# Kernel tuning notes

Hardware: AMD Instinct MI355X
Metric: run time of the kernel (lower is better)

The kernel has to match this reference:

```python
import jax, jax.numpy as jnp
import numpy as np

N_NODES = 100000
N_EDGES = 1600000
INPUT_DIM = 128
HIDDEN = 128
OUTPUT_DIM = 2
NUM_LAYERS = 2
MAX_RECURSION = 10
TAU_THRESHOLD = 0.005


def setup_inputs() -> dict:
    key = jax.random.key(0)
    ks = jax.random.split(key, 16)
    s = 0.05
    x = jax.random.normal(ks[0], (N_NODES, INPUT_DIM), dtype=jnp.float32)
    edge_index = jax.random.randint(ks[1], (2, N_EDGES), 0, N_NODES, dtype=jnp.int64)
    W_in = jax.random.normal(ks[2], (HIDDEN, INPUT_DIM), dtype=jnp.float32) * s
    b_in = jax.random.normal(ks[3], (HIDDEN,), dtype=jnp.float32) * s
    Wd = jax.random.normal(ks[4], (NUM_LAYERS, HIDDEN, 2 * HIDDEN), dtype=jnp.float32) * s
    bd = jax.random.normal(ks[5], (NUM_LAYERS, HIDDEN), dtype=jnp.float32) * s
    Wt = jax.random.normal(ks[6], (1, HIDDEN), dtype=jnp.float32) * s
    bt = jax.random.normal(ks[7], (1,), dtype=jnp.float32) * s
    W_ih = jax.random.normal(ks[8], (3 * HIDDEN, HIDDEN), dtype=jnp.float32) * s
    W_hh = jax.random.normal(ks[9], (3 * HIDDEN, HIDDEN), dtype=jnp.float32) * s
    b_ih = jax.random.normal(ks[10], (3 * HIDDEN,), dtype=jnp.float32) * s
    b_hh = jax.random.normal(ks[11], (3 * HIDDEN,), dtype=jnp.float32) * s
    Wo = jax.random.normal(ks[12], (OUTPUT_DIM, HIDDEN), dtype=jnp.float32) * s
    bo = jax.random.normal(ks[13], (OUTPUT_DIM,), dtype=jnp.float32) * s
    return dict(x=x, edge_index=edge_index, W_in=W_in, b_in=b_in, Wd=Wd, bd=bd,
                Wt=Wt, bt=bt, W_ih=W_ih, W_hh=W_hh, b_ih=b_ih, b_hh=b_hh, Wo=Wo, bo=bo)


def _gru_cell(x, h, W_ih, W_hh, b_ih, b_hh):
    # torch.nn.GRUCell math
    gi = x @ W_ih.T + b_ih  # [N, 3H]
    gh = h @ W_hh.T + b_hh
    i_r, i_z, i_n = jnp.split(gi, 3, axis=-1)
    h_r, h_z, h_n = jnp.split(gh, 3, axis=-1)
    r = jax.nn.sigmoid(i_r + h_r)
    z = jax.nn.sigmoid(i_z + h_z)
    n = jnp.tanh(i_n + r * h_n)
    return (1.0 - z) * n + z * h


def reference(x, edge_index, W_in, b_in, Wd, bd, Wt, bt, W_ih, W_hh, b_ih, b_hh, Wo, bo):
    N = x.shape[0]
    row, col = edge_index[0], edge_index[1]
    h = jax.nn.relu(x @ W_in.T + b_in)  # [N, H]
    tau = None
    for l in range(NUM_LAYERS):
        diff = jnp.abs(h[row] - h[col])  # [E, H]
        diff_agg = jax.ops.segment_sum(diff, row, num_segments=N)  # [N, H]
        h = jax.nn.relu(jnp.concatenate([h, diff_agg], axis=-1) @ Wd[l].T + bd[l])
        tau = jax.nn.softplus(h @ Wt.T + bt).squeeze(-1)  # [N]
        # n_updates = clamp(floor(1/tau), max=MAX_RECURSION); node updated iff
        # n_updates > 0 and tau < TAU_THRESHOLD. The original inner loop applies
        # gru(diff_agg[i], h[i]) with the ORIGINAL h[i] each iteration, so repeated
        # application is idempotent -> single masked GRU step is exact same math.
        n_updates = jnp.minimum(jnp.floor(1.0 / tau).astype(jnp.int32), MAX_RECURSION)
        mask = (n_updates > 0) & (tau < TAU_THRESHOLD)
        h_gru = _gru_cell(diff_agg, h, W_ih, W_hh, b_ih, b_hh)
        h = jnp.where(mask[:, None], h_gru, h)
    out = h @ Wo.T + bo  # [N, OUTPUT_DIM]
    return out, tau
```

## Files before the change

### kernel.cpp

```cpp
#include <hip/hip_runtime.h>
#include <cstdint>
#include <cstddef>

#define HID 128
#define BSHIFT 7
#define NSB 256
#define MAXB 4096

__global__ __launch_bounds__(256)
void ecount_kernel(const int* __restrict__ row, int* __restrict__ countsT,
                   int E, int nbuck,
                   const float* __restrict__ W_in, const float* __restrict__ Wd,
                   const float* __restrict__ W_ih, const float* __restrict__ W_hh,
                   float* __restrict__ WinT, float* __restrict__ WdT0,
                   float* __restrict__ WdT1, float* __restrict__ WihT,
                   float* __restrict__ WhhT) {
  for (int i = blockIdx.x * 256 + threadIdx.x; i < 180224; i += NSB * 256) {
    int j = i;
    if (j < 16384) { int r = j >> 7, c = j & 127; WinT[c * 128 + r] = W_in[j]; continue; }
    j -= 16384;
    if (j < 32768) { int r = j >> 8, c = j & 255; WdT0[c * 128 + r] = Wd[j]; continue; }
    j -= 32768;
    if (j < 32768) { int r = j >> 8, c = j & 255; WdT1[c * 128 + r] = Wd[32768 + j]; continue; }
    j -= 32768;
    if (j < 49152) { int r = j >> 7, c = j & 127; WihT[c * 384 + r] = W_ih[j]; continue; }
    j -= 49152;
    { int r = j >> 7, c = j & 127; WhhT[c * 384 + r] = W_hh[j]; }
  }
  __shared__ int lh[1024];
  int b = blockIdx.x;
  for (int i = threadIdx.x; i < nbuck; i += 256) lh[i] = 0;
  __syncthreads();
  int per = (E + NSB - 1) / NSB;
  int s = b * per, e = min(s + per, E);
  for (int i = s + (int)threadIdx.x; i < e; i += 256)
    atomicAdd(&lh[row[i] >> BSHIFT], 1);
  __syncthreads();
  for (int i = threadIdx.x; i < nbuck; i += 256) countsT[i * NSB + b] = lh[i];
}

__global__ __launch_bounds__(NSB)
void bprefix_kernel(int* __restrict__ countsT, int* __restrict__ btotal, int nbuck) {
  __shared__ int sd[NSB];
  int bk = blockIdx.x;
  int t = threadIdx.x;
  int v = countsT[bk * NSB + t];
  sd[t] = v;
  __syncthreads();
  for (int off = 1; off < NSB; off <<= 1) {
    int u = (t >= off) ? sd[t - off] : 0;
    __syncthreads();
    sd[t] += u;
    __syncthreads();
  }
  countsT[bk * NSB + t] = sd[t] - v;
  if (t == NSB - 1) btotal[bk] = sd[t];
}

__global__ __launch_bounds__(1024)
void bstart_kernel(const int* __restrict__ btotal, int* __restrict__ bstart,
                   int* __restrict__ offsets, int N, int nbuck) {
  __shared__ int sd[1024];
  int t = threadIdx.x;
  int v = (t < nbuck) ? btotal[t] : 0;
  sd[t] = v;
  __syncthreads();
  for (int off = 1; off < 1024; off <<= 1) {
    int u = (t >= off) ? sd[t - off] : 0;
    __syncthreads();
    sd[t] += u;
    __syncthreads();
  }
  if (t < nbuck) bstart[t] = sd[t] - v;
  if (t == nbuck - 1) { bstart[nbuck] = sd[t]; offsets[N] = sd[t]; }
}

__global__ __launch_bounds__(256)
void escatter_kernel(const int* __restrict__ row, const int* __restrict__ col,
                     const int* __restrict__ countsT, const int* __restrict__ bstart,
                     int2* __restrict__ ebuf, int E, int nbuck) {
  __shared__ int lcur[1024];
  int b = blockIdx.x;
  for (int i = threadIdx.x; i < nbuck; i += 256)
    lcur[i] = bstart[i] + countsT[i * NSB + b];
  __syncthreads();
  int per = (E + NSB - 1) / NSB;
  int s = b * per, e = min(s + per, E);
  for (int i = s + (int)threadIdx.x; i < e; i += 256) {
    int r = row[i], c = col[i];
    int pos = atomicAdd(&lcur[r >> BSHIFT], 1);
    ebuf[pos] = make_int2(r, c);
  }
}

__global__ __launch_bounds__(256)
void bsort_kernel(const int2* __restrict__ ebuf, const int* __restrict__ bstart,
                  int* __restrict__ offsets, int* __restrict__ csr_col,
                  int N, int nbuck) {
  __shared__ int cnt[128], off[128], cur[128];
  __shared__ int lcol[MAXB];
  int bk = blockIdx.x;
  int tid = threadIdx.x;
  int s = bstart[bk], e = bstart[bk + 1];
  int m = e - s;
  if (tid < 128) cnt[tid] = 0;
  __syncthreads();
  for (int i = s + tid; i < e; i += 256)
    atomicAdd(&cnt[ebuf[i].x & 127], 1);
  __syncthreads();
  if (tid < 128) off[tid] = cnt[tid];
  __syncthreads();
  for (int d = 1; d < 128; d <<= 1) {
    int v = 0;
    if (tid < 128 && tid >= d) v = off[tid - d];
    __syncthreads();
    if (tid < 128) off[tid] += v;
    __syncthreads();
  }
  if (tid < 128) {
    cur[tid] = off[tid] - cnt[tid];
    int node = (bk << BSHIFT) + tid;
    if (node < N) offsets[node] = s + off[tid] - cnt[tid];
  }
  __syncthreads();
  if (m <= MAXB) {
    for (int i = s + tid; i < e; i += 256) {
      int2 rc = ebuf[i];
      int pos = atomicAdd(&cur[rc.x & 127], 1);
      lcol[pos] = rc.y;
    }
    __syncthreads();
    if (tid < 128) {
      int b0 = off[tid] - cnt[tid], b1 = off[tid];
      for (int i = b0 + 1; i < b1; ++i) {
        int key = lcol[i];
        int j = i - 1;
        while (j >= b0 && lcol[j] > key) { lcol[j + 1] = lcol[j]; --j; }
        lcol[j + 1] = key;
      }
    }
    __syncthreads();
    for (int i = tid; i < m; i += 256) csr_col[s + i] = lcol[i];
  } else {
    for (int i = s + tid; i < e; i += 256) {
      int2 rc = ebuf[i];
      int pos = atomicAdd(&cur[rc.x & 127], 1);
      csr_col[s + pos] = rc.y;
    }
  }
}

__global__ __launch_bounds__(256)
void aggregate_kernel(const float* __restrict__ h, const int* __restrict__ offsets,
                      const int* __restrict__ csr_col, float* __restrict__ diff,
                      int N) {
  int wave = threadIdx.x >> 6;
  int lane = threadIdx.x & 63;
  int node = blockIdx.x * 4 + wave;
  if (node >= N) return;
  int start = offsets[node], end = offsets[node + 1];
  int deg = end - start;
  const float2* hrow = (const float2*)(h + (size_t)node * HID);
  float2 hv = hrow[lane];
  float a0 = 0.f, a1 = 0.f;

  int batch = min(deg, 64);
  int myc = (lane < batch) ? csr_col[start + lane] : 0;
  int j = 0;
  for (; j + 16 <= batch; j += 16) {
    const float2* p0 = (const float2*)(h + (size_t)__shfl(myc, j + 0) * HID);
    const float2* p1 = (const float2*)(h + (size_t)__shfl(myc, j + 1) * HID);
    const float2* p2 = (const float2*)(h + (size_t)__shfl(myc, j + 2) * HID);
    const float2* p3 = (const float2*)(h + (size_t)__shfl(myc, j + 3) * HID);
    const float2* p4 = (const float2*)(h + (size_t)__shfl(myc, j + 4) * HID);
    const float2* p5 = (const float2*)(h + (size_t)__shfl(myc, j + 5) * HID);
    const float2* p6 = (const float2*)(h + (size_t)__shfl(myc, j + 6) * HID);
    const float2* p7 = (const float2*)(h + (size_t)__shfl(myc, j + 7) * HID);
    const float2* q0 = (const float2*)(h + (size_t)__shfl(myc, j + 8) * HID);
    const float2* q1 = (const float2*)(h + (size_t)__shfl(myc, j + 9) * HID);
    const float2* q2 = (const float2*)(h + (size_t)__shfl(myc, j + 10) * HID);
    const float2* q3 = (const float2*)(h + (size_t)__shfl(myc, j + 11) * HID);
    const float2* q4 = (const float2*)(h + (size_t)__shfl(myc, j + 12) * HID);
    const float2* q5 = (const float2*)(h + (size_t)__shfl(myc, j + 13) * HID);
    const float2* q6 = (const float2*)(h + (size_t)__shfl(myc, j + 14) * HID);
    const float2* q7 = (const float2*)(h + (size_t)__shfl(myc, j + 15) * HID);
    float2 x0 = p0[lane], x1 = p1[lane], x2 = p2[lane], x3 = p3[lane];
    float2 x4 = p4[lane], x5 = p5[lane], x6 = p6[lane], x7 = p7[lane];
    float2 y0 = q0[lane], y1 = q1[lane], y2 = q2[lane], y3 = q3[lane];
    float2 y4 = q4[lane], y5 = q5[lane], y6 = q6[lane], y7 = q7[lane];
    a0 += fabsf(hv.x - x0.x) + fabsf(hv.x - x1.x) + fabsf(hv.x - x2.x) + fabsf(hv.x - x3.x)
        + fabsf(hv.x - x4.x) + fabsf(hv.x - x5.x) + fabsf(hv.x - x6.x) + fabsf(hv.x - x7.x);
    a1 += fabsf(hv.y - x0.y) + fabsf(hv.y - x1.y) + fabsf(hv.y - x2.y) + fabsf(hv.y - x3.y)
        + fabsf(hv.y - x4.y) + fabsf(hv.y - x5.y) + fabsf(hv.y - x6.y) + fabsf(hv.y - x7.y);
    a0 += fabsf(hv.x - y0.x) + fabsf(hv.x - y1.x) + fabsf(hv.x - y2.x) + fabsf(hv.x - y3.x)
        + fabsf(hv.x - y4.x) + fabsf(hv.x - y5.x) + fabsf(hv.x - y6.x) + fabsf(hv.x - y7.x);
    a1 += fabsf(hv.y - y0.y) + fabsf(hv.y - y1.y) + fabsf(hv.y - y2.y) + fabsf(hv.y - y3.y)
        + fabsf(hv.y - y4.y) + fabsf(hv.y - y5.y) + fabsf(hv.y - y6.y) + fabsf(hv.y - y7.y);
  }
  for (; j + 8 <= batch; j += 8) {
    const float2* p0 = (const float2*)(h + (size_t)__shfl(myc, j + 0) * HID);
    const float2* p1 = (const float2*)(h + (size_t)__shfl(myc, j + 1) * HID);
    const float2* p2 = (const float2*)(h + (size_t)__shfl(myc, j + 2) * HID);
    const float2* p3 = (const float2*)(h + (size_t)__shfl(myc, j + 3) * HID);
    const float2* p4 = (const float2*)(h + (size_t)__shfl(myc, j + 4) * HID);
    const float2* p5 = (const float2*)(h + (size_t)__shfl(myc, j + 5) * HID);
    const float2* p6 = (const float2*)(h + (size_t)__shfl(myc, j + 6) * HID);
    const float2* p7 = (const float2*)(h + (size_t)__shfl(myc, j + 7) * HID);
    float2 x0 = p0[lane], x1 = p1[lane], x2 = p2[lane], x3 = p3[lane];
    float2 x4 = p4[lane], x5 = p5[lane], x6 = p6[lane], x7 = p7[lane];
    a0 += fabsf(hv.x - x0.x) + fabsf(hv.x - x1.x) + fabsf(hv.x - x2.x) + fabsf(hv.x - x3.x)
        + fabsf(hv.x - x4.x) + fabsf(hv.x - x5.x) + fabsf(hv.x - x6.x) + fabsf(hv.x - x7.x);
    a1 += fabsf(hv.y - x0.y) + fabsf(hv.y - x1.y) + fabsf(hv.y - x2.y) + fabsf(hv.y - x3.y)
        + fabsf(hv.y - x4.y) + fabsf(hv.y - x5.y) + fabsf(hv.y - x6.y) + fabsf(hv.y - x7.y);
  }
  for (; j < batch; ++j) {
    const float2* p = (const float2*)(h + (size_t)__shfl(myc, j) * HID);
    float2 x = p[lane];
    a0 += fabsf(hv.x - x.x);
    a1 += fabsf(hv.y - x.y);
  }
  for (int e = start + 64; e < end; ++e) {
    const float2* p = (const float2*)(h + (size_t)csr_col[e] * HID);
    float2 x = p[lane];
    a0 += fabsf(hv.x - x.x);
    a1 += fabsf(hv.y - x.y);
  }
  *(float2*)(diff + (size_t)node * HID + 2 * lane) = make_float2(a0, a1);
}

template<bool TAU>
__global__ __launch_bounds__(256)
void gemm_kernel(const float* __restrict__ A1, const float* __restrict__ A2,
                 const float* __restrict__ BT, const float* __restrict__ bias,
                 float* __restrict__ C, int M, int nchunks,
                 const float* __restrict__ Wt, const float* __restrict__ bt,
                 float* __restrict__ tau_out, int* __restrict__ mlist,
                 int* __restrict__ mcount) {
  __shared__ float As[32][68];
  __shared__ float Bs[32][128];
  __shared__ float taured[64];
  int tid = threadIdx.x;
  int tx = tid & 31;
  int ty = tid >> 5;
  int i0 = blockIdx.x * 64;
  float acc[8][4] = {};

  for (int kc = 0; kc < nchunks; ++kc) {
    const float* A = (kc < 4) ? A1 : A2;
    int ksrc = (kc & 3) * 32;
    int kglob = kc * 32;
    #pragma unroll
    for (int q = 0; q < 2; ++q) {
      int f = q * 256 + tid;
      int i = f >> 3;
      int kq = (f & 7) << 2;
      int ig = i0 + i; if (ig >= M) ig = M - 1;
      float4 v = *(const float4*)(A + (size_t)ig * HID + ksrc + kq);
      As[kq + 0][i] = v.x; As[kq + 1][i] = v.y;
      As[kq + 2][i] = v.z; As[kq + 3][i] = v.w;
    }
    #pragma unroll
    for (int q = 0; q < 4; ++q) {
      int f = q * 256 + tid;
      int k = f >> 5; int c4 = (f & 31) << 2;
      *(float4*)&Bs[k][c4] = *(const float4*)(BT + (size_t)(kglob + k) * HID + c4);
    }
    __syncthreads();
    #pragma unroll
    for (int k = 0; k < 32; ++k) {
      float a[8];
      const float4* ap = (const float4*)&As[k][ty * 8];
      float4 a0 = ap[0], a1 = ap[1];
      a[0]=a0.x; a[1]=a0.y; a[2]=a0.z; a[3]=a0.w;
      a[4]=a1.x; a[5]=a1.y; a[6]=a1.z; a[7]=a1.w;
      float4 b4 = *(const float4*)&Bs[k][tx * 4];
      #pragma unroll
      for (int r = 0; r < 8; ++r) {
        acc[r][0] = fmaf(a[r], b4.x, acc[r][0]);
        acc[r][1] = fmaf(a[r], b4.y, acc[r][1]);
        acc[r][2] = fmaf(a[r], b4.z, acc[r][2]);
        acc[r][3] = fmaf(a[r], b4.w, acc[r][3]);
      }
    }
    __syncthreads();
  }

  float4 bias4 = *(const float4*)(bias + tx * 4);
  float bias_r[4] = {bias4.x, bias4.y, bias4.z, bias4.w};
  float wt_r[4] = {0.f, 0.f, 0.f, 0.f};
  if constexpr (TAU) {
    float4 w4 = *(const float4*)(Wt + tx * 4);
    wt_r[0] = w4.x; wt_r[1] = w4.y; wt_r[2] = w4.z; wt_r[3] = w4.w;
  }
  #pragma unroll
  for (int r = 0; r < 8; ++r) {
    int row = i0 + ty * 8 + r;
    bool ok = row < M;
    float v0 = fmaxf(acc[r][0] + bias_r[0], 0.f);
    float v1 = fmaxf(acc[r][1] + bias_r[1], 0.f);
    float v2 = fmaxf(acc[r][2] + bias_r[2], 0.f);
    float v3 = fmaxf(acc[r][3] + bias_r[3], 0.f);
    if (ok) {
      float4 v4 = make_float4(v0, v1, v2, v3);
      *(float4*)(C + (size_t)row * HID + tx * 4) = v4;
    }
    if constexpr (TAU) {
      float p = v0 * wt_r[0];
      p = fmaf(v1, wt_r[1], p);
      p = fmaf(v2, wt_r[2], p);
      p = fmaf(v3, wt_r[3], p);
      p += __shfl_down(p, 16, 32);
      p += __shfl_down(p, 8, 32);
      p += __shfl_down(p, 4, 32);
      p += __shfl_down(p, 2, 32);
      p += __shfl_down(p, 1, 32);
      if (tx == 0) taured[ty * 8 + r] = p;
    }
  }
  if constexpr (TAU) {
    __syncthreads();
    if (tid < 64) {
      int row = i0 + tid;
      if (row < M) {
        float pre = taured[tid] + bt[0];
        float tau = (pre > 20.f) ? pre : log1pf(expf(pre));
        tau_out[row] = tau;
        if (tau < 0.005f && (1.0f / tau) < 2147483648.0f) {
          int pos = atomicAdd(mcount, 1);
          mlist[pos] = row;
        }
      }
    }
  }
}

__global__ __launch_bounds__(512)
void gru_kernel(const float* __restrict__ diff, float* __restrict__ h,
                const int* __restrict__ list, const int* __restrict__ count,
                const float* __restrict__ WihT, const float* __restrict__ WhhT,
                const float* __restrict__ b_ih, const float* __restrict__ b_hh) {
  int cnt = *count;
  int base = blockIdx.x * 32;
  if (base >= cnt) return;
  __shared__ float dl[32][HID];
  __shared__ float hl[32][HID];
  __shared__ int ids[32];
  int tid = threadIdx.x;
  if (tid < 32) ids[tid] = (base + tid < cnt) ? list[base + tid] : -1;
  __syncthreads();
  #pragma unroll
  for (int q = 0; q < 8; ++q) {
    int f = q * 512 + tid;
    int r = f >> 7, c = f & 127;
    int id = ids[r];
    int src = (id >= 0) ? id : 0;
    dl[r][c] = diff[(size_t)src * HID + c];
    hl[r][c] = h[(size_t)src * HID + c];
  }
  __syncthreads();
  int tx = tid & 127, ty = tid >> 7;
  float air[8] = {}, aiz[8] = {}, ain[8] = {}, ahr[8] = {}, ahz[8] = {}, ahn[8] = {};
  for (int k = 0; k < HID; ++k) {
    float wir = WihT[k * 384 + tx];
    float wiz = WihT[k * 384 + 128 + tx];
    float win = WihT[k * 384 + 256 + tx];
    float whr = WhhT[k * 384 + tx];
    float whz = WhhT[k * 384 + 128 + tx];
    float whn = WhhT[k * 384 + 256 + tx];
    #pragma unroll
    for (int r = 0; r < 8; ++r) {
      float dk = dl[ty * 8 + r][k];
      float hk = hl[ty * 8 + r][k];
      air[r] = fmaf(dk, wir, air[r]);
      aiz[r] = fmaf(dk, wiz, aiz[r]);
      ain[r] = fmaf(dk, win, ain[r]);
      ahr[r] = fmaf(hk, whr, ahr[r]);
      ahz[r] = fmaf(hk, whz, ahz[r]);
      ahn[r] = fmaf(hk, whn, ahn[r]);
    }
  }
  float bir = b_ih[tx], biz = b_ih[128 + tx], bin = b_ih[256 + tx];
  float bhr = b_hh[tx], bhz = b_hh[128 + tx], bhn = b_hh[256 + tx];
  #pragma unroll
  for (int r = 0; r < 8; ++r) {
    int id = ids[ty * 8 + r];
    if (id < 0) continue;
    float rg = 1.f / (1.f + expf(-((air[r] + bir) + (ahr[r] + bhr))));
    float z  = 1.f / (1.f + expf(-((aiz[r] + biz) + (ahz[r] + bhz))));
    float n  = tanhf((ain[r] + bin) + rg * (ahn[r] + bhn));
    float hv = hl[ty * 8 + r][tx];
    h[(size_t)id * HID + tx] = (1.f - z) * n + z * hv;
  }
}

__global__ void out_kernel(const float* __restrict__ h, const float* __restrict__ Wo,
                           const float* __restrict__ bo, float* __restrict__ out, int N) {
  int g = blockIdx.x * blockDim.x + threadIdx.x;
  int node = g >> 5;
  int sub = threadIdx.x & 31;
  if (node >= N) return;
  float4 hv = *(const float4*)(h + (size_t)node * HID + sub * 4);
  float4 w0 = *(const float4*)(Wo + sub * 4);
  float4 w1 = *(const float4*)(Wo + 128 + sub * 4);
  float s0 = hv.x * w0.x + hv.y * w0.y + hv.z * w0.z + hv.w * w0.w;
  float s1 = hv.x * w1.x + hv.y * w1.y + hv.z * w1.z + hv.w * w1.w;
  for (int d = 16; d; d >>= 1) {
    s0 += __shfl_down(s0, d, 32);
    s1 += __shfl_down(s1, d, 32);
  }
  if (sub == 0) {
    out[(size_t)node * 2 + 0] = s0 + bo[0];
    out[(size_t)node * 2 + 1] = s1 + bo[1];
  }
}

extern "C" void kernel_launch(void* const* d_in, const int* in_sizes, int n_in,
                              void* d_out, int out_size, void* d_ws, size_t ws_size,
                              hipStream_t stream) {
  const float* x    = (const float*)d_in[0];
  const int*   ei   = (const int*)d_in[1];
  const float* W_in = (const float*)d_in[2];
  const float* b_in = (const float*)d_in[3];
  const float* Wd   = (const float*)d_in[4];
  const float* bd   = (const float*)d_in[5];
  const float* Wt   = (const float*)d_in[6];
  const float* bt   = (const float*)d_in[7];
  const float* W_ih = (const float*)d_in[8];
  const float* W_hh = (const float*)d_in[9];
  const float* b_ih = (const float*)d_in[10];
  const float* b_hh = (const float*)d_in[11];
  const float* Wo   = (const float*)d_in[12];
  const float* bo   = (const float*)d_in[13];

  const int N = in_sizes[0] / HID;
  const int E = in_sizes[1] / 2;
  const int* rowp = ei;
  const int* colp = ei + E;
  const int nbuck = (N + (1 << BSHIFT) - 1) >> BSHIFT;

  char* p = (char*)d_ws;
  auto alloc = [&](size_t bytes) { void* r = (void*)p; p += (bytes + 255) & ~(size_t)255; return r; };
  float* hA     = (float*)alloc((size_t)N * HID * 4);
  float* hB     = (float*)alloc((size_t)N * HID * 4);
  float* diff   = (float*)alloc((size_t)N * HID * 4);
  float* WinT   = (float*)alloc(128 * 128 * 4);
  float* WdT0   = (float*)alloc(256 * 128 * 4);
  float* WdT1   = (float*)alloc(256 * 128 * 4);
  float* WihT   = (float*)alloc(128 * 384 * 4);
  float* WhhT   = (float*)alloc(128 * 384 * 4);
  float* tau0   = (float*)alloc((size_t)N * 4);
  int*   list   = (int*)alloc((size_t)N * 4);
  int*   count  = (int*)alloc(256);
  int*   countsT= (int*)alloc((size_t)1024 * NSB * 4);
  int*   btotal = (int*)alloc(1024 * 4);
  int*   bstart = (int*)alloc(1028 * 4);
  int*   offs   = (int*)alloc(((size_t)N + 1) * 4);
  int*   csrcol = (int*)alloc((size_t)E * 4);
  int2*  ebuf   = (int2*)alloc((size_t)E * 8);

  float* out_ptr = (float*)d_out;
  float* tau_out = (float*)d_out + (size_t)N * 2;

  hipMemsetAsync(count, 0, 8, stream);

  ecount_kernel<<<NSB, 256, 0, stream>>>(rowp, countsT, E, nbuck,
                                         W_in, Wd, W_ih, W_hh,
                                         WinT, WdT0, WdT1, WihT, WhhT);
  bprefix_kernel<<<nbuck, NSB, 0, stream>>>(countsT, btotal, nbuck);
  bstart_kernel<<<1, 1024, 0, stream>>>(btotal, bstart, offs, N, nbuck);
  escatter_kernel<<<NSB, 256, 0, stream>>>(rowp, colp, countsT, bstart, ebuf, E, nbuck);
  bsort_kernel<<<nbuck, 256, 0, stream>>>(ebuf, bstart, offs, csrcol, N, nbuck);

  const int gemm_blocks = (N + 63) / 64;
  const int agg_blocks = (N + 3) / 4;
  const int gru_blocks = (N + 31) / 32;

  gemm_kernel<false><<<gemm_blocks, 256, 0, stream>>>(
      x, nullptr, WinT, b_in, hA, N, 4, nullptr, nullptr, nullptr, nullptr, nullptr);

  aggregate_kernel<<<agg_blocks, 256, 0, stream>>>(hA, offs, csrcol, diff, N);
  gemm_kernel<true><<<gemm_blocks, 256, 0, stream>>>(
      hA, diff, WdT0, bd, hB, N, 8, Wt, bt, tau0, list, count);
  gru_kernel<<<gru_blocks, 512, 0, stream>>>(diff, hB, list, count, WihT, WhhT, b_ih, b_hh);

  aggregate_kernel<<<agg_blocks, 256, 0, stream>>>(hB, offs, csrcol, diff, N);
  gemm_kernel<true><<<gemm_blocks, 256, 0, stream>>>(
      hB, diff, WdT1, bd + 128, hA, N, 8, Wt, bt, tau_out, list, count + 1);
  gru_kernel<<<gru_blocks, 512, 0, stream>>>(diff, hA, list, count + 1, WihT, WhhT, b_ih, b_hh);

  out_kernel<<<((size_t)N * 32 + 255) / 256, 256, 0, stream>>>(hA, Wo, bo, out_ptr, N);
}
```

Measured before the change: 737.6 us.

## Fuse neighbor aggregation into layer GEMM and fold output projection into epilogues

The separate aggregate kernel is replaced by an aggregation phase inside each layer GEMM block: each block computes the diff rows for its 64 nodes into shared memory and uses them directly as the second half of the K dimension, so those rows no longer have to be reread from global memory. The output projection kernel is removed. It is now computed in the last layer GEMM epilogue for all nodes and recomputed in the final GRU kernel for the nodes that GRU updates. The fused kernel uses about 52KB of shared memory, which lowers occupancy during the latency-bound gather phase. Diff is still written to global memory because the GRU needs it.

Result: slower. 866.6 us (+17.5%).

```diff
diff --git a/kernel.cpp b/kernel.cpp
--- a/kernel.cpp
+++ b/kernel.cpp
@@ -6,6 +6,7 @@
 #define BSHIFT 7
 #define NSB 256
 #define MAXB 4096
+
 
 __global__ __launch_bounds__(256)
 void ecount_kernel(const int* __restrict__ row, int* __restrict__ countsT,
@@ -151,104 +152,17 @@
 }
 
 __global__ __launch_bounds__(256)
-void aggregate_kernel(const float* __restrict__ h, const int* __restrict__ offsets,
-                      const int* __restrict__ csr_col, float* __restrict__ diff,
-                      int N) {
-  int wave = threadIdx.x >> 6;
-  int lane = threadIdx.x & 63;
-  int node = blockIdx.x * 4 + wave;
-  if (node >= N) return;
-  int start = offsets[node], end = offsets[node + 1];
-  int deg = end - start;
-  const float2* hrow = (const float2*)(h + (size_t)node * HID);
-  float2 hv = hrow[lane];
-  float a0 = 0.f, a1 = 0.f;
-
-  int batch = min(deg, 64);
-  int myc = (lane < batch) ? csr_col[start + lane] : 0;
-  int j = 0;
-  for (; j + 16 <= batch; j += 16) {
-    const float2* p0 = (const float2*)(h + (size_t)__shfl(myc, j + 0) * HID);
-    const float2* p1 = (const float2*)(h + (size_t)__shfl(myc, j + 1) * HID);
-    const float2* p2 = (const float2*)(h + (size_t)__shfl(myc, j + 2) * HID);
-    const float2* p3 = (const float2*)(h + (size_t)__shfl(myc, j + 3) * HID);
-    const float2* p4 = (const float2*)(h + (size_t)__shfl(myc, j + 4) * HID);
-    const float2* p5 = (const float2*)(h + (size_t)__shfl(myc, j + 5) * HID);
-    const float2* p6 = (const float2*)(h + (size_t)__shfl(myc, j + 6) * HID);
-    const float2* p7 = (const float2*)(h + (size_t)__shfl(myc, j + 7) * HID);
-    const float2* q0 = (const float2*)(h + (size_t)__shfl(myc, j + 8) * HID);
-    const float2* q1 = (const float2*)(h + (size_t)__shfl(myc, j + 9) * HID);
-    const float2* q2 = (const float2*)(h + (size_t)__shfl(myc, j + 10) * HID);
-    const float2* q3 = (const float2*)(h + (size_t)__shfl(myc, j + 11) * HID);
-    const float2* q4 = (const float2*)(h + (size_t)__shfl(myc, j + 12) * HID);
-    const float2* q5 = (const float2*)(h + (size_t)__shfl(myc, j + 13) * HID);
-    const float2* q6 = (const float2*)(h + (size_t)__shfl(myc, j + 14) * HID);
-    const float2* q7 = (const float2*)(h + (size_t)__shfl(myc, j + 15) * HID);
-    float2 x0 = p0[lane], x1 = p1[lane], x2 = p2[lane], x3 = p3[lane];
-    float2 x4 = p4[lane], x5 = p5[lane], x6 = p6[lane], x7 = p7[lane];
-    float2 y0 = q0[lane], y1 = q1[lane], y2 = q2[lane], y3 = q3[lane];
-    float2 y4 = q4[lane], y5 = q5[lane], y6 = q6[lane], y7 = q7[lane];
-    a0 += fabsf(hv.x - x0.x) + fabsf(hv.x - x1.x) + fabsf(hv.x - x2.x) + fabsf(hv.x - x3.x)
-        + fabsf(hv.x - x4.x) + fabsf(hv.x - x5.x) + fabsf(hv.x - x6.x) + fabsf(hv.x - x7.x);
-    a1 += fabsf(hv.y - x0.y) + fabsf(hv.y - x1.y) + fabsf(hv.y - x2.y) + fabsf(hv.y - x3.y)
-        + fabsf(hv.y - x4.y) + fabsf(hv.y - x5.y) + fabsf(hv.y - x6.y) + fabsf(hv.y - x7.y);
-    a0 += fabsf(hv.x - y0.x) + fabsf(hv.x - y1.x) + fabsf(hv.x - y2.x) + fabsf(hv.x - y3.x)
-        + fabsf(hv.x - y4.x) + fabsf(hv.x - y5.x) + fabsf(hv.x - y6.x) + fabsf(hv.x - y7.x);
-    a1 += fabsf(hv.y - y0.y) + fabsf(hv.y - y1.y) + fabsf(hv.y - y2.y) + fabsf(hv.y - y3.y)
-        + fabsf(hv.y - y4.y) + fabsf(hv.y - y5.y) + fabsf(hv.y - y6.y) + fabsf(hv.y - y7.y);
-  }
-  for (; j + 8 <= batch; j += 8) {
-    const float2* p0 = (const float2*)(h + (size_t)__shfl(myc, j + 0) * HID);
-    const float2* p1 = (const float2*)(h + (size_t)__shfl(myc, j + 1) * HID);
-    const float2* p2 = (const float2*)(h + (size_t)__shfl(myc, j + 2) * HID);
-    const float2* p3 = (const float2*)(h + (size_t)__shfl(myc, j + 3) * HID);
-    const float2* p4 = (const float2*)(h + (size_t)__shfl(myc, j + 4) * HID);
-    const float2* p5 = (const float2*)(h + (size_t)__shfl(myc, j + 5) * HID);
-    const float2* p6 = (const float2*)(h + (size_t)__shfl(myc, j + 6) * HID);
-    const float2* p7 = (const float2*)(h + (size_t)__shfl(myc, j + 7) * HID);
-    float2 x0 = p0[lane], x1 = p1[lane], x2 = p2[lane], x3 = p3[lane];
-    float2 x4 = p4[lane], x5 = p5[lane], x6 = p6[lane], x7 = p7[lane];
-    a0 += fabsf(hv.x - x0.x) + fabsf(hv.x - x1.x) + fabsf(hv.x - x2.x) + fabsf(hv.x - x3.x)
-        + fabsf(hv.x - x4.x) + fabsf(hv.x - x5.x) + fabsf(hv.x - x6.x) + fabsf(hv.x - x7.x);
-    a1 += fabsf(hv.y - x0.y) + fabsf(hv.y - x1.y) + fabsf(hv.y - x2.y) + fabsf(hv.y - x3.y)
-        + fabsf(hv.y - x4.y) + fabsf(hv.y - x5.y) + fabsf(hv.y - x6.y) + fabsf(hv.y - x7.y);
-  }
-  for (; j < batch; ++j) {
-    const float2* p = (const float2*)(h + (size_t)__shfl(myc, j) * HID);
-    float2 x = p[lane];
-    a0 += fabsf(hv.x - x.x);
-    a1 += fabsf(hv.y - x.y);
-  }
-  for (int e = start + 64; e < end; ++e) {
-    const float2* p = (const float2*)(h + (size_t)csr_col[e] * HID);
-    float2 x = p[lane];
-    a0 += fabsf(hv.x - x.x);
-    a1 += fabsf(hv.y - x.y);
-  }
-  *(float2*)(diff + (size_t)node * HID + 2 * lane) = make_float2(a0, a1);
-}
-
-template<bool TAU>
-__global__ __launch_bounds__(256)
-void gemm_kernel(const float* __restrict__ A1, const float* __restrict__ A2,
-                 const float* __restrict__ BT, const float* __restrict__ bias,
-                 float* __restrict__ C, int M, int nchunks,
-                 const float* __restrict__ Wt, const float* __restrict__ bt,
-                 float* __restrict__ tau_out, int* __restrict__ mlist,
-                 int* __restrict__ mcount) {
+void gemm_in_kernel(const float* __restrict__ A, const float* __restrict__ BT,
+                    const float* __restrict__ bias, float* __restrict__ C, int M) {
   __shared__ float As[32][68];
   __shared__ float Bs[32][128];
-  __shared__ float taured[64];
   int tid = threadIdx.x;
   int tx = tid & 31;
   int ty = tid >> 5;
   int i0 = blockIdx.x * 64;
   float acc[8][4] = {};
-
-  for (int kc = 0; kc < nchunks; ++kc) {
-    const float* A = (kc < 4) ? A1 : A2;
-    int ksrc = (kc & 3) * 32;
-    int kglob = kc * 32;
+  for (int kc = 0; kc < 4; ++kc) {
+    int ksrc = kc * 32;
     #pragma unroll
     for (int q = 0; q < 2; ++q) {
       int f = q * 256 + tid;
@@ -263,7 +177,7 @@
     for (int q = 0; q < 4; ++q) {
       int f = q * 256 + tid;
       int k = f >> 5; int c4 = (f & 31) << 2;
-      *(float4*)&Bs[k][c4] = *(const float4*)(BT + (size_t)(kglob + k) * HID + c4);
+      *(float4*)&Bs[k][c4] = *(const float4*)(BT + (size_t)(ksrc + k) * HID + c4);
     }
     __syncthreads();
     #pragma unroll
@@ -284,13 +198,171 @@
     }
     __syncthreads();
   }
+  float4 bias4 = *(const float4*)(bias + tx * 4);
+  #pragma unroll
+  for (int r = 0; r < 8; ++r) {
+    int row = i0 + ty * 8 + r;
+    if (row >= M) continue;
+    float4 v4 = make_float4(fmaxf(acc[r][0] + bias4.x, 0.f),
+                            fmaxf(acc[r][1] + bias4.y, 0.f),
+                            fmaxf(acc[r][2] + bias4.z, 0.f),
+                            fmaxf(acc[r][3] + bias4.w, 0.f));
+    *(float4*)(C + (size_t)row * HID + tx * 4) = v4;
+  }
+}
+
+template<bool OUT>
+__global__ __launch_bounds__(256)
+void fgemm_kernel(const float* __restrict__ h, const float* __restrict__ BT,
+                  const float* __restrict__ bias, float* __restrict__ C,
+                  const int* __restrict__ offsets, const int* __restrict__ csr_col,
+                  float* __restrict__ diffG, int M,
+                  const float* __restrict__ Wt, const float* __restrict__ bt,
+                  float* __restrict__ tau_out, int* __restrict__ mlist,
+                  int* __restrict__ mcount,
+                  const float* __restrict__ Wo, const float* __restrict__ bo,
+                  float* __restrict__ outp) {
+  __shared__ float As[32][68];
+  __shared__ float Bs[32][128];
+  __shared__ float dL[128][68];
+  __shared__ float taured[64];
+  int tid = threadIdx.x;
+  int i0 = blockIdx.x * 64;
+
+  {
+    int wave = tid >> 6;
+    int lane = tid & 63;
+    for (int t = 0; t < 16; ++t) {
+      int nl = wave * 16 + t;
+      int node = i0 + nl;
+      if (node >= M) break;
+      int start = offsets[node], end = offsets[node + 1];
+      int deg = end - start;
+      const float2* hrow = (const float2*)(h + (size_t)node * HID);
+      float2 hv = hrow[lane];
+      float a0 = 0.f, a1 = 0.f;
+      int batch = min(deg, 64);
+      int myc = (lane < batch) ? csr_col[start + lane] : 0;
+      int j = 0;
+      for (; j + 16 <= batch; j += 16) {
+        const float2* p0 = (const float2*)(h + (size_t)__shfl(myc, j + 0) * HID);
+        const float2* p1 = (const float2*)(h + (size_t)__shfl(myc, j + 1) * HID);
+        const float2* p2 = (const float2*)(h + (size_t)__shfl(myc, j + 2) * HID);
+        const float2* p3 = (const float2*)(h + (size_t)__shfl(myc, j + 3) * HID);
+        const float2* p4 = (const float2*)(h + (size_t)__shfl(myc, j + 4) * HID);
+        const float2* p5 = (const float2*)(h + (size_t)__shfl(myc, j + 5) * HID);
+        const float2* p6 = (const float2*)(h + (size_t)__shfl(myc, j + 6) * HID);
+        const float2* p7 = (const float2*)(h + (size_t)__shfl(myc, j + 7) * HID);
+        const float2* q0 = (const float2*)(h + (size_t)__shfl(myc, j + 8) * HID);
+        const float2* q1 = (const float2*)(h + (size_t)__shfl(myc, j + 9) * HID);
+        const float2* q2 = (const float2*)(h + (size_t)__shfl(myc, j + 10) * HID);
+        const float2* q3 = (const float2*)(h + (size_t)__shfl(myc, j + 11) * HID);
+        const float2* q4 = (const float2*)(h + (size_t)__shfl(myc, j + 12) * HID);
+        const float2* q5 = (const float2*)(h + (size_t)__shfl(myc, j + 13) * HID);
+        const float2* q6 = (const float2*)(h + (size_t)__shfl(myc, j + 14) * HID);
+        const float2* q7 = (const float2*)(h + (size_t)__shfl(myc, j + 15) * HID);
+        float2 x0 = p0[lane], x1 = p1[lane], x2 = p2[lane], x3 = p3[lane];
+        float2 x4 = p4[lane], x5 = p5[lane], x6 = p6[lane], x7 = p7[lane];
+        float2 y0 = q0[lane], y1 = q1[lane], y2 = q2[lane], y3 = q3[lane];
+        float2 y4 = q4[lane], y5 = q5[lane], y6 = q6[lane], y7 = q7[lane];
+        a0 += fabsf(hv.x - x0.x) + fabsf(hv.x - x1.x) + fabsf(hv.x - x2.x) + fabsf(hv.x - x3.x)
+            + fabsf(hv.x - x4.x) + fabsf(hv.x - x5.x) + fabsf(hv.x - x6.x) + fabsf(hv.x - x7.x);
+        a1 += fabsf(hv.y - x0.y) + fabsf(hv.y - x1.y) + fabsf(hv.y - x2.y) + fabsf(hv.y - x3.y)
+            + fabsf(hv.y - x4.y) + fabsf(hv.y - x5.y) + fabsf(hv.y - x6.y) + fabsf(hv.y - x7.y);
+        a0 += fabsf(hv.x - y0.x) + fabsf(hv.x - y1.x) + fabsf(hv.x - y2.x) + fabsf(hv.x - y3.x)
+            + fabsf(hv.x - y4.x) + fabsf(hv.x - y5.x) + fabsf(hv.x - y6.x) + fabsf(hv.x - y7.x);
+        a1 += fabsf(hv.y - y0.y) + fabsf(hv.y - y1.y) + fabsf(hv.y - y2.y) + fabsf(hv.y - y3.y)
+            + fabsf(hv.y - y4.y) + fabsf(hv.y - y5.y) + fabsf(hv.y - y6.y) + fabsf(hv.y - y7.y);
+      }
+      for (; j + 8 <= batch; j += 8) {
+        const float2* p0 = (const float2*)(h + (size_t)__shfl(myc, j + 0) * HID);
+        const float2* p1 = (const float2*)(h + (size_t)__shfl(myc, j + 1) * HID);
+        const float2* p2 = (const float2*)(h + (size_t)__shfl(myc, j + 2) * HID);
+        const float2* p3 = (const float2*)(h + (size_t)__shfl(myc, j + 3) * HID);
+        const float2* p4 = (const float2*)(h + (size_t)__shfl(myc, j + 4) * HID);
+        const float2* p5 = (const float2*)(h + (size_t)__shfl(myc, j + 5) * HID);
+        const float2* p6 = (const float2*)(h + (size_t)__shfl(myc, j + 6) * HID);
+        const float2* p7 = (const float2*)(h + (size_t)__shfl(myc, j + 7) * HID);
+        float2 x0 = p0[lane], x1 = p1[lane], x2 = p2[lane], x3 = p3[lane];
+        float2 x4 = p4[lane], x5 = p5[lane], x6 = p6[lane], x7 = p7[lane];
+        a0 += fabsf(hv.x - x0.x) + fabsf(hv.x - x1.x) + fabsf(hv.x - x2.x) + fabsf(hv.x - x3.x)
+            + fabsf(hv.x - x4.x) + fabsf(hv.x - x5.x) + fabsf(hv.x - x6.x) + fabsf(hv.x - x7.x);
+        a1 += fabsf(hv.y - x0.y) + fabsf(hv.y - x1.y) + fabsf(hv.y - x2.y) + fabsf(hv.y - x3.y)
+            + fabsf(hv.y - x4.y) + fabsf(hv.y - x5.y) + fabsf(hv.y - x6.y) + fabsf(hv.y - x7.y);
+      }
+      for (; j < batch; ++j) {
+        const float2* p = (const float2*)(h + (size_t)__shfl(myc, j) * HID);
+        float2 x = p[lane];
+        a0 += fabsf(hv.x - x.x);
+        a1 += fabsf(hv.y - x.y);
+      }
+      for (int e2 = start + 64; e2 < end; ++e2) {
+        const float2* p = (const float2*)(h + (size_t)csr_col[e2] * HID);
+        float2 x = p[lane];
+        a0 += fabsf(hv.x - x.x);
+        a1 += fabsf(hv.y - x.y);
+      }
+      *(float2*)(diffG + (size_t)node * HID + 2 * lane) = make_float2(a0, a1);
+      dL[2 * lane][nl] = a0;
+      dL[2 * lane + 1][nl] = a1;
+    }
+  }
+  __syncthreads();
+
+  int tx = tid & 31;
+  int ty = tid >> 5;
+  float acc[8][4] = {};
+  for (int kc = 0; kc < 8; ++kc) {
+    if (kc < 4) {
+      int ksrc = kc * 32;
+      #pragma unroll
+      for (int q = 0; q < 2; ++q) {
+        int f = q * 256 + tid;
+        int i = f >> 3;
+        int kq = (f & 7) << 2;
+        int ig = i0 + i; if (ig >= M) ig = M - 1;
+        float4 v = *(const float4*)(h + (size_t)ig * HID + ksrc + kq);
+        As[kq + 0][i] = v.x; As[kq + 1][i] = v.y;
+        As[kq + 2][i] = v.z; As[kq + 3][i] = v.w;
+      }
+    }
+    int kglob = kc * 32;
+    #pragma unroll
+    for (int q = 0; q < 4; ++q) {
+      int f = q * 256 + tid;
+      int k = f >> 5; int c4 = (f & 31) << 2;
+      *(float4*)&Bs[k][c4] = *(const float4*)(BT + (size_t)(kglob + k) * HID + c4);
+    }
+    __syncthreads();
+    const float (*Asrc)[68] = (kc < 4) ? As : (const float (*)[68])&dL[(kc - 4) * 32];
+    #pragma unroll
+    for (int k = 0; k < 32; ++k) {
+      float a[8];
+      const float4* ap = (const float4*)&Asrc[k][ty * 8];
+      float4 a0 = ap[0], a1 = ap[1];
+      a[0]=a0.x; a[1]=a0.y; a[2]=a0.z; a[3]=a0.w;
+      a[4]=a1.x; a[5]=a1.y; a[6]=a1.z; a[7]=a1.w;
+      float4 b4 = *(const float4*)&Bs[k][tx * 4];
+      #pragma unroll
+      for (int r = 0; r < 8; ++r) {
+        acc[r][0] = fmaf(a[r], b4.x, acc[r][0]);
+        acc[r][1] = fmaf(a[r], b4.y, acc[r][1]);
+        acc[r][2] = fmaf(a[r], b4.z, acc[r][2]);
+        acc[r][3] = fmaf(a[r], b4.w, acc[r][3]);
+      }
+    }
+    __syncthreads();
+  }
 
   float4 bias4 = *(const float4*)(bias + tx * 4);
   float bias_r[4] = {bias4.x, bias4.y, bias4.z, bias4.w};
-  float wt_r[4] = {0.f, 0.f, 0.f, 0.f};
-  if constexpr (TAU) {
-    float4 w4 = *(const float4*)(Wt + tx * 4);
-    wt_r[0] = w4.x; wt_r[1] = w4.y; wt_r[2] = w4.z; wt_r[3] = w4.w;
+  float4 w4 = *(const float4*)(Wt + tx * 4);
+  float wt_r[4] = {w4.x, w4.y, w4.z, w4.w};
+  float4 wo0 = make_float4(0.f, 0.f, 0.f, 0.f);
+  float4 wo1 = make_float4(0.f, 0.f, 0.f, 0.f);
+  if constexpr (OUT) {
+    wo0 = *(const float4*)(Wo + tx * 4);
+    wo1 = *(const float4*)(Wo + 128 + tx * 4);
   }
   #pragma unroll
   for (int r = 0; r < 8; ++r) {
@@ -304,47 +376,62 @@
       float4 v4 = make_float4(v0, v1, v2, v3);
       *(float4*)(C + (size_t)row * HID + tx * 4) = v4;
     }
-    if constexpr (TAU) {
-      float p = v0 * wt_r[0];
-      p = fmaf(v1, wt_r[1], p);
-      p = fmaf(v2, wt_r[2], p);
-      p = fmaf(v3, wt_r[3], p);
-      p += __shfl_down(p, 16, 32);
-      p += __shfl_down(p, 8, 32);
-      p += __shfl_down(p, 4, 32);
-      p += __shfl_down(p, 2, 32);
-      p += __shfl_down(p, 1, 32);
-      if (tx == 0) taured[ty * 8 + r] = p;
-    }
-  }
-  if constexpr (TAU) {
-    __syncthreads();
-    if (tid < 64) {
-      int row = i0 + tid;
-      if (row < M) {
-        float pre = taured[tid] + bt[0];
-        float tau = (pre > 20.f) ? pre : log1pf(expf(pre));
-        tau_out[row] = tau;
-        if (tau < 0.005f && (1.0f / tau) < 2147483648.0f) {
-          int pos = atomicAdd(mcount, 1);
-          mlist[pos] = row;
-        }
-      }
-    }
-  }
-}
-
+    if constexpr (OUT) {
+      float o0 = v0 * wo0.x + v1 * wo0.y + v2 * wo0.z + v3 * wo0.w;
+      float o1 = v0 * wo1.x + v1 * wo1.y + v2 * wo1.z + v3 * wo1.w;
+      o0 += __shfl_down(o0, 16, 32); o1 += __shfl_down(o1, 16, 32);
+      o0 += __shfl_down(o0, 8, 32);  o1 += __shfl_down(o1, 8, 32);
+      o0 += __shfl_down(o0, 4, 32);  o1 += __shfl_down(o1, 4, 32);
+      o0 += __shfl_down(o0, 2, 32);  o1 += __shfl_down(o1, 2, 32);
+      o0 += __shfl_down(o0, 1, 32);  o1 += __shfl_down(o1, 1, 32);
+      if (tx == 0 && ok) {
+        outp[(size_t)row * 2 + 0] = o0 + bo[0];
+        outp[(size_t)row * 2 + 1] = o1 + bo[1];
+      }
+    }
+    {
+      float pf = v0 * wt_r[0];
+      pf = fmaf(v1, wt_r[1], pf);
+      pf = fmaf(v2, wt_r[2], pf);
+      pf = fmaf(v3, wt_r[3], pf);
+      pf += __shfl_down(pf, 16, 32);
+      pf += __shfl_down(pf, 8, 32);
+      pf += __shfl_down(pf, 4, 32);
+      pf += __shfl_down(pf, 2, 32);
+      pf += __shfl_down(pf, 1, 32);
+      if (tx == 0) taured[ty * 8 + r] = pf;
+    }
+  }
+  __syncthreads();
+  if (tid < 64) {
+    int row = i0 + tid;
+    if (row < M) {
+      float pre = taured[tid] + bt[0];
+      float tau = (pre > 20.f) ? pre : log1pf(expf(pre));
+      tau_out[row] = tau;
+      if (tau < 0.005f && (1.0f / tau) < 2147483648.0f) {
+        int pos = atomicAdd(mcount, 1);
+        mlist[pos] = row;
+      }
+    }
+  }
+}
+
+template<bool LAST>
 __global__ __launch_bounds__(512)
 void gru_kernel(const float* __restrict__ diff, float* __restrict__ h,
                 const int* __restrict__ list, const int* __restrict__ count,
                 const float* __restrict__ WihT, const float* __restrict__ WhhT,
-                const float* __restrict__ b_ih, const float* __restrict__ b_hh) {
+                const float* __restrict__ b_ih, const float* __restrict__ b_hh,
+                const float* __restrict__ Wo, const float* __restrict__ bo,
+                float* __restrict__ outp) {
   int cnt = *count;
   int base = blockIdx.x * 32;
   if (base >= cnt) return;
   __shared__ float dl[32][HID];
   __shared__ float hl[32][HID];
   __shared__ int ids[32];
+  __shared__ float osum[32][2][2];
   int tid = threadIdx.x;
   if (tid < 32) ids[tid] = (base + tid < cnt) ? list[base + tid] : -1;
   __syncthreads();
@@ -381,36 +468,41 @@
   }
   float bir = b_ih[tx], biz = b_ih[128 + tx], bin = b_ih[256 + tx];
   float bhr = b_hh[tx], bhz = b_hh[128 + tx], bhn = b_hh[256 + tx];
+  float wol0 = 0.f, wol1 = 0.f;
+  if constexpr (LAST) { wol0 = Wo[tx]; wol1 = Wo[128 + tx]; }
   #pragma unroll
   for (int r = 0; r < 8; ++r) {
     int id = ids[ty * 8 + r];
-    if (id < 0) continue;
     float rg = 1.f / (1.f + expf(-((air[r] + bir) + (ahr[r] + bhr))));
     float z  = 1.f / (1.f + expf(-((aiz[r] + biz) + (ahz[r] + bhz))));
     float n  = tanhf((ain[r] + bin) + rg * (ahn[r] + bhn));
     float hv = hl[ty * 8 + r][tx];
-    h[(size_t)id * HID + tx] = (1.f - z) * n + z * hv;
-  }
-}
-
-__global__ void out_kernel(const float* __restrict__ h, const float* __restrict__ Wo,
-                           const float* __restrict__ bo, float* __restrict__ out, int N) {
-  int g = blockIdx.x * blockDim.x + threadIdx.x;
-  int node = g >> 5;
-  int sub = threadIdx.x & 31;
-  if (node >= N) return;
-  float4 hv = *(const float4*)(h + (size_t)node * HID + sub * 4);
-  float4 w0 = *(const float4*)(Wo + sub * 4);
-  float4 w1 = *(const float4*)(Wo + 128 + sub * 4);
-  float s0 = hv.x * w0.x + hv.y * w0.y + hv.z * w0.z + hv.w * w0.w;
-  float s1 = hv.x * w1.x + hv.y * w1.y + hv.z * w1.z + hv.w * w1.w;
-  for (int d = 16; d; d >>= 1) {
-    s0 += __shfl_down(s0, d, 32);
-    s1 += __shfl_down(s1, d, 32);
-  }
-  if (sub == 0) {
-    out[(size_t)node * 2 + 0] = s0 + bo[0];
-    out[(size_t)node * 2 + 1] = s1 + bo[1];
+    float hnew = (1.f - z) * n + z * hv;
+    if (id >= 0) h[(size_t)id * HID + tx] = hnew;
+    if constexpr (LAST) {
+      float p0 = hnew * wol0;
+      float p1 = hnew * wol1;
+      p0 += __shfl_down(p0, 32, 64); p1 += __shfl_down(p1, 32, 64);
+      p0 += __shfl_down(p0, 16, 64); p1 += __shfl_down(p1, 16, 64);
+      p0 += __shfl_down(p0, 8, 64);  p1 += __shfl_down(p1, 8, 64);
+      p0 += __shfl_down(p0, 4, 64);  p1 += __shfl_down(p1, 4, 64);
+      p0 += __shfl_down(p0, 2, 64);  p1 += __shfl_down(p1, 2, 64);
+      p0 += __shfl_down(p0, 1, 64);  p1 += __shfl_down(p1, 1, 64);
+      if ((tx & 63) == 0) {
+        osum[ty * 8 + r][tx >> 6][0] = p0;
+        osum[ty * 8 + r][tx >> 6][1] = p1;
+      }
+    }
+  }
+  if constexpr (LAST) {
+    __syncthreads();
+    if (tid < 32) {
+      int id = ids[tid];
+      if (id >= 0) {
+        outp[(size_t)id * 2 + 0] = osum[tid][0][0] + osum[tid][1][0] + bo[0];
+        outp[(size_t)id * 2 + 1] = osum[tid][0][1] + osum[tid][1][1] + bo[1];
+      }
+    }
   }
 }
 
@@ -472,21 +564,19 @@
   bsort_kernel<<<nbuck, 256, 0, stream>>>(ebuf, bstart, offs, csrcol, N, nbuck);
 
   const int gemm_blocks = (N + 63) / 64;
-  const int agg_blocks = (N + 3) / 4;
   const int gru_blocks = (N + 31) / 32;
 
-  gemm_kernel<false><<<gemm_blocks, 256, 0, stream>>>(
-      x, nullptr, WinT, b_in, hA, N, 4, nullptr, nullptr, nullptr, nullptr, nullptr);
-
-  aggregate_kernel<<<agg_blocks, 256, 0, stream>>>(hA, offs, csrcol, diff, N);
-  gemm_kernel<true><<<gemm_blocks, 256, 0, stream>>>(
-      hA, diff, WdT0, bd, hB, N, 8, Wt, bt, tau0, list, count);
-  gru_kernel<<<gru_blocks, 512, 0, stream>>>(diff, hB, list, count, WihT, WhhT, b_ih, b_hh);
-
-  aggregate_kernel<<<agg_blocks, 256, 0, stream>>>(hB, offs, csrcol, diff, N);
-  gemm_kernel<true><<<gemm_blocks, 256, 0, stream>>>(
-      hB, diff, WdT1, bd + 128, hA, N, 8, Wt, bt, tau_out, list, count + 1);
-  gru_kernel<<<gru_blocks, 512, 0, stream>>>(diff, hA, list, count + 1, WihT, WhhT, b_ih, b_hh);
-
-  out_kernel<<<((size_t)N * 32 + 255) / 256, 256, 0, stream>>>(hA, Wo, bo, out_ptr, N);
-}
+  gemm_in_kernel<<<gemm_blocks, 256, 0, stream>>>(x, WinT, b_in, hA, N);
+
+  fgemm_kernel<false><<<gemm_blocks, 256, 0, stream>>>(
+      hA, WdT0, bd, hB, offs, csrcol, diff, N,
+      Wt, bt, tau0, list, count, nullptr, nullptr, nullptr);
+  gru_kernel<false><<<gru_blocks, 512, 0, stream>>>(
+      diff, hB, list, count, WihT, WhhT, b_ih, b_hh, nullptr, nullptr, nullptr);
+
+  fgemm_kernel<true><<<gemm_blocks, 256, 0, stream>>>(
+      hB, WdT1, bd + 128, hA, offs, csrcol, diff, N,
+      Wt, bt, tau_out, list, count + 1, Wo, bo, out_ptr);
+  gru_kernel<true><<<gru_blocks, 512, 0, stream>>>(
+      diff, hA, list, count + 1, WihT, WhhT, b_ih, b_hh, Wo, bo, out_ptr);
+}
```
